# Optimization experiments

Hardware: AMD Instinct MI355X
Metric: run time of the kernel (lower is better)

Reference implementation:

```python
import jax, jax.numpy as jnp
import numpy as np

B, S, E, C = 128, 256, 768, 4


def setup_inputs() -> dict:
    key = jax.random.key(0)
    ks = jax.random.split(key, 8)
    questions = jax.random.normal(ks[0], (B, E), dtype=jnp.float32)
    segments = jax.random.normal(ks[1], (B, S, E), dtype=jnp.float32)
    W1 = jax.random.normal(ks[2], (2 * E, E), dtype=jnp.float32) * 0.02
    b1 = jnp.zeros((E,), dtype=jnp.float32)
    W2 = jax.random.normal(ks[3], (E, E // 2), dtype=jnp.float32) * 0.02
    b2 = jnp.zeros((E // 2,), dtype=jnp.float32)
    W3 = jax.random.normal(ks[4], (E // 2, C), dtype=jnp.float32) * 0.02
    b3 = jnp.zeros((C,), dtype=jnp.float32)
    num_segments = jax.random.randint(ks[5], (B,), 1, S + 1, dtype=jnp.int32)
    return {"questions": questions, "segments": segments, "W1": W1, "b1": b1,
            "W2": W2, "b2": b2, "W3": W3, "b3": b3, "num_segments": num_segments}


def reference(questions, segments, W1, b1, W2, b2, W3, b3, num_segments):
    # --- MLP instance scores (call()): concat question emb with every segment emb ---
    q = jnp.broadcast_to(questions[:, None, :], segments.shape)      # [B,S,E]
    x = jnp.concatenate([q, segments], axis=-1)                      # [B,S,2E]
    h = jax.nn.gelu(x @ W1 + b1, approximate=False)                  # keras gelu is exact
    h = jax.nn.gelu(h @ W2 + b2, approximate=False)
    preds = jax.nn.softmax(h @ W3 + b3, axis=-1)                     # [B,S,C]

    # --- per-bag noisy-OR style aggregation (aggregate_loss inner math, vectorized) ---
    # In the TF code, for class cid: s_j = sum(preds[j,:cid]) (exclusive cumsum over
    # classes), and product_of_sum_prob ACCUMULATES across the i loop, so
    # update_i = preds[i,cid] * cumprod_i( prod_{j!=k} s_j ) (leave-one-out products).
    mask = jnp.arange(S)[None, :] < num_segments[:, None]            # [B,S]
    mC = mask[..., None]                                             # [B,S,1]
    s = jnp.cumsum(preds, axis=-1) - preds                           # exclusive cumsum, [B,S,C]
    s_m = jnp.where(mC, s, 1.0)                                      # padded -> multiplicative identity
    # leave-one-out product over the segment axis via prefix/suffix cumprods
    cp_f = jnp.cumprod(s_m, axis=1)
    prefix = jnp.concatenate([jnp.ones_like(s_m[:, :1]), cp_f[:, :-1]], axis=1)
    cp_b = jnp.cumprod(s_m[:, ::-1], axis=1)[:, ::-1]
    suffix = jnp.concatenate([cp_b[:, 1:], jnp.ones_like(s_m[:, :1])], axis=1)
    L = prefix * suffix                                              # prod_{j!=k} s_j, [B,S,C]
    cpL = jnp.cumprod(L, axis=1)                                     # running product over i (padding is at the end)
    sum_term = jnp.sum(jnp.where(mC, preds * cpL, 0.0), axis=1)      # [B,C]
    prod_term = jnp.prod(jnp.where(mC, preds, 1.0), axis=1)          # prod_i preds[i,cid]
    agg = sum_term / jnp.float32(C) + prod_term                      # bag_pred_agg_scores, [B,C]
    return agg
```

## Files before the change

### kernel.cpp

```cpp
#include <hip/hip_runtime.h>
#include <hip/hip_bf16.h>


typedef __attribute__((ext_vector_type(8))) short short8;
typedef __attribute__((ext_vector_type(8))) unsigned short ushort8;
typedef __attribute__((ext_vector_type(16))) float f32x16;
typedef __attribute__((ext_vector_type(8))) int i32x8;
typedef __attribute__((ext_vector_type(4))) int i32x4;

__device__ __forceinline__ unsigned short f2bf(float f) {
    union { float f; unsigned int u; } c; c.f = f;
    unsigned int u = c.u;
    unsigned int r = (u + 0x7FFFu + ((u >> 16) & 1u)) >> 16;
    return (unsigned short)r;
}
__device__ __forceinline__ float bf2f(unsigned short u) {
    union { unsigned int u; float f; } c; c.u = ((unsigned int)u) << 16;
    return c.f;
}
__device__ __forceinline__ float gelu_fast(float x) {
    float x2 = x * x;
    float y2 = 1.5957691216057308f * (x + 0.044715f * x2 * x);
    float e = __expf(y2);
    float t = 1.0f - 2.0f * __builtin_amdgcn_rcpf(e + 1.0f);
    return 0.5f * x * (1.0f + t);
}

typedef const __attribute__((address_space(1))) void* gas_t;
typedef __attribute__((address_space(3))) void* las_t;
__device__ __forceinline__ void g2l16(const void* g, void* l) {
    __builtin_amdgcn_global_load_lds((gas_t)g, (las_t)l, 16, 0, 0);
}

__device__ __forceinline__ unsigned int f4_to_fp8x4(float a, float b, float c, float d) {
    int lo = __builtin_amdgcn_cvt_pk_fp8_f32(a, b, 0, 0);
    return (unsigned int)__builtin_amdgcn_cvt_pk_fp8_f32(c, d, lo, 1);
}
__device__ __forceinline__ unsigned char f_to_fp8(float a) {
    return (unsigned char)(__builtin_amdgcn_cvt_pk_fp8_f32(a, a, 0, 0) & 0xFF);
}

#define PREP_Q    96
#define PREP_TR1E 240
#define PREP_TR2E 312
#define PREP_END  12600

__global__ __launch_bounds__(256) void prep_kernel(
    const float* __restrict__ segments, unsigned char* __restrict__ segF8,
    const float* __restrict__ W1, unsigned char* __restrict__ W1t8,
    const float* __restrict__ W2, unsigned char* __restrict__ W2t8,
    const float* __restrict__ questions, float* __restrict__ qW1p)
{
    __shared__ __align__(16) char sh[16640];
    const int bid = blockIdx.x, tid = threadIdx.x;

    if (bid < PREP_Q) {
        const int s = bid / 24, rem = bid % 24;
        const int n0 = (rem % 12) * 64, m0 = (rem / 12) * 64;
        float (*As)[64] = (float(*)[64])sh;
        float (*Bs)[64] = (float(*)[64])(sh + 4096);
        const int tn = tid & 15, tm = tid >> 4;
        float acc[4][4] = {};
        const int la_m = tid >> 2;
        const int la_k = (tid & 3) << 2;
        const int lb_k = tid >> 4;
        const int lb_n = (tid & 15) << 2;
        const float* Aptr = questions + (size_t)(m0 + la_m) * 768 + la_k;
        const float* Bptr = W1 + (size_t)lb_k * 768 + n0 + lb_n;
        const int kbeg = s * 192, kend = kbeg + 192;
        for (int k0 = kbeg; k0 < kend; k0 += 16) {
            float4 av = *(const float4*)(Aptr + k0);
            float4 bv = *(const float4*)(Bptr + (size_t)k0 * 768);
            As[la_k + 0][la_m] = av.x;
            As[la_k + 1][la_m] = av.y;
            As[la_k + 2][la_m] = av.z;
            As[la_k + 3][la_m] = av.w;
            *(float4*)&Bs[lb_k][lb_n] = bv;
            __syncthreads();
            #pragma unroll
            for (int k = 0; k < 16; k++) {
                float4 a = *(const float4*)&As[k][tm << 2];
                float4 b = *(const float4*)&Bs[k][tn << 2];
                float ar[4] = {a.x, a.y, a.z, a.w};
                float br[4] = {b.x, b.y, b.z, b.w};
                #pragma unroll
                for (int i = 0; i < 4; i++)
                    #pragma unroll
                    for (int j = 0; j < 4; j++)
                        acc[i][j] += ar[i] * br[j];
            }
            __syncthreads();
        }
        float* outp = qW1p + (size_t)s * 128 * 768;
        #pragma unroll
        for (int i = 0; i < 4; i++) {
            int row = m0 + (tm << 2) + i;
            int colBase = n0 + (tn << 2);
            *(float4*)&outp[(size_t)row * 768 + colBase] =
                make_float4(acc[i][0], acc[i][1], acc[i][2], acc[i][3]);
        }
        return;
    }

    if (bid < PREP_TR2E) {
        const float* in; unsigned char* outp; int R, C, bx, by;
        if (bid < PREP_TR1E) {
            int idx = bid - PREP_Q; bx = idx % 12; by = idx / 12;
            in = W1 + 768 * 768; outp = W1t8; R = 768; C = 768;
        } else {
            int idx = bid - PREP_TR1E; bx = idx % 6; by = idx / 6;
            in = W2; outp = W2t8; R = 768; C = 384;
        }
        float (*t)[65] = (float(*)[65])sh;
        int r0 = by * 64, c0 = bx * 64;
        int tx = tid & 63, ty = tid >> 6;
        #pragma unroll
        for (int p = 0; p < 16; p++) {
            int row = ty * 16 + p;
            t[row][tx] = in[(size_t)(r0 + row) * C + c0 + tx];
        }
        __syncthreads();
        #pragma unroll
        for (int p = 0; p < 16; p++) {
            int orow = ty * 16 + p;
            outp[(size_t)(c0 + orow) * R + r0 + tx] = f_to_fp8(t[tx][orow]);
        }
        return;
    }

    {
        long i = (long)(bid - PREP_TR2E) * 256 + tid;
        const float4* in = (const float4*)segments;
        float4 a = in[2 * i], b = in[2 * i + 1];
        unsigned int lo = f4_to_fp8x4(a.x, a.y, a.z, a.w);
        unsigned int hi = f4_to_fp8x4(b.x, b.y, b.z, b.w);
        *(uint2*)(segF8 + i * 8) = make_uint2(lo, hi);
    }
}

template<int OUT8>
__global__ __launch_bounds__(256) void mfma_gemm_f8(
    const unsigned char* __restrict__ A8,
    const unsigned char* __restrict__ Bt8,
    const float* __restrict__ bias,
    const float* __restrict__ rowAdd,
    void* __restrict__ CoutV,
    int M, int N, int K)
{
    __shared__ __align__(16) unsigned char smem8[32768];
    unsigned char* As = smem8;
    unsigned char* Bs = smem8 + 8192;
    const int tid = threadIdx.x;
    const int wave = tid >> 6, lane = tid & 63;
    const int m0 = blockIdx.y * 128, n0 = blockIdx.x * 128;
    const int wm = (wave & 1) * 64, wn = (wave >> 1) * 64;

    f32x16 acc[2][2] = {};

    const int srow = tid >> 2;
    const int schunk = (tid & 3) ^ ((srow >> 1) & 3);
    const unsigned char* Ag = A8 + (size_t)(m0 + srow) * K + schunk * 16;
    const unsigned char* Bg = Bt8 + (size_t)(n0 + srow) * K + schunk * 16;
    unsigned char* Al = As + tid * 16;
    unsigned char* Bl = Bs + tid * 16;

    const int fm = lane & 31, fq = lane >> 5;

    for (int k0 = 0; k0 < K; k0 += 64) {
        g2l16(Ag + k0, Al);
        g2l16(Ag + (size_t)64 * K + k0, Al + 4096);
        g2l16(Bg + k0, Bl);
        g2l16(Bg + (size_t)64 * K + k0, Bl + 4096);
        __syncthreads();

        i32x8 av[2], bv[2];
        #pragma unroll
        for (int i = 0; i < 2; i++) {
            int rw = wm + i * 32 + fm, key = (rw >> 1) & 3;
            i32x4 lo = *(const i32x4*)&As[rw * 64 + (((fq << 1) | 0) ^ key) * 16];
            i32x4 hi = *(const i32x4*)&As[rw * 64 + (((fq << 1) | 1) ^ key) * 16];
            av[i][0] = lo[0]; av[i][1] = lo[1]; av[i][2] = lo[2]; av[i][3] = lo[3];
            av[i][4] = hi[0]; av[i][5] = hi[1]; av[i][6] = hi[2]; av[i][7] = hi[3];
        }
        #pragma unroll
        for (int j = 0; j < 2; j++) {
            int rw = wn + j * 32 + fm, key = (rw >> 1) & 3;
            i32x4 lo = *(const i32x4*)&Bs[rw * 64 + (((fq << 1) | 0) ^ key) * 16];
            i32x4 hi = *(const i32x4*)&Bs[rw * 64 + (((fq << 1) | 1) ^ key) * 16];
            bv[j][0] = lo[0]; bv[j][1] = lo[1]; bv[j][2] = lo[2]; bv[j][3] = lo[3];
            bv[j][4] = hi[0]; bv[j][5] = hi[1]; bv[j][6] = hi[2]; bv[j][7] = hi[3];
        }
        #pragma unroll
        for (int i = 0; i < 2; i++)
            #pragma unroll
            for (int j = 0; j < 2; j++)
                acc[i][j] = __builtin_amdgcn_mfma_scale_f32_32x32x64_f8f6f4(
                    av[i], bv[j], acc[i][j], 0, 0,
                    0, 127, 0, 127);
        __syncthreads();
    }

    #pragma unroll
    for (int j = 0; j < 2; j++) {
        int coll = wn + j * 32 + fm;
        int col = n0 + coll;
        float add = bias[col];
        if (rowAdd) {
            const float* radd = rowAdd + (size_t)(m0 >> 8) * N;
            add += radd[col] + radd[col + 98304] +
                   radd[col + 2 * 98304] + radd[col + 3 * 98304];
        }
        #pragma unroll
        for (int i = 0; i < 2; i++) {
            int rbase = wm + i * 32 + 4 * fq;
            #pragma unroll
            for (int reg = 0; reg < 16; reg++) {
                int rowl = rbase + (reg & 3) + 8 * (reg >> 2);
                float v = gelu_fast(acc[i][j][reg] + add);
                if (OUT8) smem8[rowl * 128 + coll] = f_to_fp8(v);
                else ((unsigned short*)smem8)[rowl * 128 + coll] = f2bf(v);
            }
        }
    }
    __syncthreads();
    if (OUT8) {
        unsigned char* Cout = (unsigned char*)CoutV;
        #pragma unroll
        for (int it = 0; it < 4; it++) {
            int idx = it * 256 + tid;
            int r = idx >> 3, cc = (idx & 7) * 16;
            *(uint4*)&Cout[(size_t)(m0 + r) * N + n0 + cc] =
                *(const uint4*)&smem8[r * 128 + cc];
        }
    } else {
        unsigned short* Cout = (unsigned short*)CoutV;
        #pragma unroll
        for (int it = 0; it < 8; it++) {
            int idx = it * 256 + tid;
            int r = idx >> 4, cc = (idx & 15) * 8;
            *(ushort8*)&Cout[(size_t)(m0 + r) * N + n0 + cc] =
                *(const ushort8*)&((unsigned short*)smem8)[r * 128 + cc];
        }
    }
}

__device__ __forceinline__ float4 f4mul(float4 a, float4 b) {
    return make_float4(a.x * b.x, a.y * b.y, a.z * b.z, a.w * b.w);
}
__device__ float4 scan_prod(float4 v, float4* buf, int tid) {
    __syncthreads();
    buf[tid] = v;
    __syncthreads();
    #pragma unroll
    for (int off = 1; off < 256; off <<= 1) {
        float4 o = (tid >= off) ? buf[tid - off] : make_float4(1.f, 1.f, 1.f, 1.f);
        __syncthreads();
        v = f4mul(v, o);
        buf[tid] = v;
        __syncthreads();
    }
    return v;
}

__global__ __launch_bounds__(256) void head_kernel(
    const unsigned short* __restrict__ H2, const float* __restrict__ W3,
    const float* __restrict__ b3, const int* __restrict__ nseg,
    float* __restrict__ out)
{
    __shared__ float4 buf[256];
    __shared__ float4 w3s[384];
    const int b = blockIdx.x, tid = threadIdx.x;
    for (int i = tid; i < 384; i += 256) w3s[i] = ((const float4*)W3)[i];
    __syncthreads();

    const unsigned short* hrow = H2 + (size_t)(b * 256 + tid) * 384;
    float4 acc = make_float4(b3[0], b3[1], b3[2], b3[3]);
    #pragma unroll
    for (int kk = 0; kk < 48; kk++) {
        ushort8 u = *(const ushort8*)(hrow + kk * 8);
        #pragma unroll
        for (int j = 0; j < 8; j++) {
            float h = bf2f(u[j]);
            float4 w = w3s[kk * 8 + j];
            acc.x += h * w.x; acc.y += h * w.y; acc.z += h * w.z; acc.w += h * w.w;
        }
    }
    float m = fmaxf(fmaxf(acc.x, acc.y), fmaxf(acc.z, acc.w));
    float e0 = __expf(acc.x - m), e1 = __expf(acc.y - m),
          e2 = __expf(acc.z - m), e3 = __expf(acc.w - m);
    float inv = 1.0f / (e0 + e1 + e2 + e3);
    float4 p = make_float4(e0 * inv, e1 * inv, e2 * inv, e3 * inv);

    const int n = nseg[b];
    const float4 ones = make_float4(1.f, 1.f, 1.f, 1.f);
    bool msk = tid < n;
    float s1 = p.x, s2 = s1 + p.y, s3 = s2 + p.z;
    float4 sm = msk ? make_float4(0.f, s1, s2, s3) : ones;

    scan_prod(sm, buf, tid);
    float4 pfx = (tid > 0) ? buf[tid - 1] : ones;
    __syncthreads();

    buf[255 - tid] = sm;
    __syncthreads();
    float4 rsm = buf[tid];
    scan_prod(rsm, buf, tid);
    float4 sfx = (tid < 255) ? buf[254 - tid] : ones;

    float4 L = f4mul(pfx, sfx);
    float4 cpL = scan_prod(L, buf, tid);

    float4 term = msk ? f4mul(p, cpL) : make_float4(0.f, 0.f, 0.f, 0.f);
    float4 pm = msk ? p : ones;

    __syncthreads();
    buf[tid] = term;
    __syncthreads();
    for (int off = 128; off > 0; off >>= 1) {
        if (tid < off) {
            float4 a = buf[tid], c = buf[tid + off];
            buf[tid] = make_float4(a.x + c.x, a.y + c.y, a.z + c.z, a.w + c.w);
        }
        __syncthreads();
    }
    float4 sum_t = buf[0];
    __syncthreads();

    buf[tid] = pm;
    __syncthreads();
    for (int off = 128; off > 0; off >>= 1) {
        if (tid < off) buf[tid] = f4mul(buf[tid], buf[tid + off]);
        __syncthreads();
    }
    if (tid == 0) {
        float4 pr = buf[0];
        ((float4*)out)[b] = make_float4(0.25f * sum_t.x + pr.x,
                                        0.25f * sum_t.y + pr.y,
                                        0.25f * sum_t.z + pr.z,
                                        0.25f * sum_t.w + pr.w);
    }
}

extern "C" void kernel_launch(void* const* d_in, const int* in_sizes, int n_in,
                              void* d_out, int out_size, void* d_ws, size_t ws_size,
                              hipStream_t stream) {
    (void)in_sizes; (void)n_in; (void)out_size; (void)ws_size;
    const float* questions = (const float*)d_in[0];
    const float* segments  = (const float*)d_in[1];
    const float* W1 = (const float*)d_in[2];
    const float* b1 = (const float*)d_in[3];
    const float* W2 = (const float*)d_in[4];
    const float* b2 = (const float*)d_in[5];
    const float* W3 = (const float*)d_in[6];
    const float* b3 = (const float*)d_in[7];
    const int*  nseg = (const int*)d_in[8];
    float* out = (float*)d_out;

    char* w = (char*)d_ws;
    float* qW1p = (float*)w;                   w += (size_t)4 * 128 * 768 * 4;
    unsigned char*  W1t8 = (unsigned char*)w;  w += (size_t)768 * 768;
    unsigned char*  W2t8 = (unsigned char*)w;  w += (size_t)384 * 768;
    unsigned char*  segF8 = (unsigned char*)w; w += (size_t)32768 * 768;
    unsigned char*  H1f8 = (unsigned char*)w;  w += (size_t)32768 * 768;
    unsigned short* H2b  = (unsigned short*)w; w += (size_t)32768 * 384 * 2;

    prep_kernel<<<PREP_END, 256, 0, stream>>>(
        segments, segF8, W1, W1t8, W2, W2t8, questions, qW1p);
    mfma_gemm_f8<1><<<dim3(6, 256), 256, 0, stream>>>(
        segF8, W1t8, b1, qW1p, H1f8, 32768, 768, 768);
    mfma_gemm_f8<0><<<dim3(3, 256), 256, 0, stream>>>(
        H1f8, W2t8, b2, nullptr, H2b, 32768, 384, 768);
    head_kernel<<<128, 256, 0, stream>>>(H2b, W3, b3, nseg, out);
}
```

Baseline: 247.7 us.

## Fuse W3 projection into second GEMM epilogue and use wave-shuffle scans in head

The second GEMM now multiplies its bf16 output tile by the matching slice of W3 inside the epilogue and writes per-column-block partial logits (3 partials of 4 floats per row) instead of the full 32768x384 bf16 H2 matrix. The head kernel sums the three partials and no longer reads H2 or performs the 384-long dot products. The shared-memory Hillis-Steele product scans and tree reductions are replaced with wave shuffle scans and reductions plus a small cross-wave combine, cutting barriers. In exchange, the GEMM epilogue gains extra LDS reads and FMAs per block.

Result: no change. 243.9 us (-1.5%).

```diff
diff --git a/kernel.cpp b/kernel.cpp
--- a/kernel.cpp
+++ b/kernel.cpp
@@ -138,22 +138,28 @@
     }
 }
 
-template<int OUT8>
+template<int MODE>
 __global__ __launch_bounds__(256) void mfma_gemm_f8(
     const unsigned char* __restrict__ A8,
     const unsigned char* __restrict__ Bt8,
     const float* __restrict__ bias,
     const float* __restrict__ rowAdd,
     void* __restrict__ CoutV,
-    int M, int N, int K)
+    int M, int N, int K,
+    const float* __restrict__ W3p)
 {
-    __shared__ __align__(16) unsigned char smem8[32768];
+    __shared__ __align__(16) unsigned char smem8[32768 + (MODE == 2 ? 2048 : 0)];
     unsigned char* As = smem8;
     unsigned char* Bs = smem8 + 8192;
     const int tid = threadIdx.x;
     const int wave = tid >> 6, lane = tid & 63;
     const int m0 = blockIdx.y * 128, n0 = blockIdx.x * 128;
     const int wm = (wave & 1) * 64, wn = (wave >> 1) * 64;
+
+    if constexpr (MODE == 2) {
+        if (tid < 128)
+            ((float4*)(smem8 + 32768))[tid] = ((const float4*)W3p)[n0 + tid];
+    }
 
     f32x16 acc[2][2] = {};
 
@@ -217,13 +223,13 @@
             for (int reg = 0; reg < 16; reg++) {
                 int rowl = rbase + (reg & 3) + 8 * (reg >> 2);
                 float v = gelu_fast(acc[i][j][reg] + add);
-                if (OUT8) smem8[rowl * 128 + coll] = f_to_fp8(v);
+                if constexpr (MODE == 1) smem8[rowl * 128 + coll] = f_to_fp8(v);
                 else ((unsigned short*)smem8)[rowl * 128 + coll] = f2bf(v);
             }
         }
     }
     __syncthreads();
-    if (OUT8) {
+    if constexpr (MODE == 1) {
         unsigned char* Cout = (unsigned char*)CoutV;
         #pragma unroll
         for (int it = 0; it < 4; it++) {
@@ -232,6 +238,28 @@
             *(uint4*)&Cout[(size_t)(m0 + r) * N + n0 + cc] =
                 *(const uint4*)&smem8[r * 128 + cc];
         }
+    } else if constexpr (MODE == 2) {
+        const float4* w3sh = (const float4*)(smem8 + 32768);
+        const unsigned short* tile = (const unsigned short*)smem8;
+        int r = tid >> 1, ch = tid & 1;
+        const unsigned short* rowp = tile + r * 128 + ch * 64;
+        float4 a = make_float4(0.f, 0.f, 0.f, 0.f);
+        #pragma unroll
+        for (int k = 0; k < 8; k++) {
+            int kk = k ^ (r & 7);
+            ushort8 u = *(const ushort8*)(rowp + kk * 8);
+            #pragma unroll
+            for (int jj = 0; jj < 8; jj++) {
+                float h = bf2f(u[jj]);
+                float4 wv2 = w3sh[ch * 64 + kk * 8 + jj];
+                a.x += h * wv2.x; a.y += h * wv2.y;
+                a.z += h * wv2.z; a.w += h * wv2.w;
+            }
+        }
+        a.x += __shfl_xor(a.x, 1); a.y += __shfl_xor(a.y, 1);
+        a.z += __shfl_xor(a.z, 1); a.w += __shfl_xor(a.w, 1);
+        if (ch == 0)
+            ((float4*)CoutV)[(size_t)blockIdx.x * 32768 + m0 + r] = a;
     } else {
         unsigned short* Cout = (unsigned short*)CoutV;
         #pragma unroll
@@ -247,44 +275,45 @@
 __device__ __forceinline__ float4 f4mul(float4 a, float4 b) {
     return make_float4(a.x * b.x, a.y * b.y, a.z * b.z, a.w * b.w);
 }
-__device__ float4 scan_prod(float4 v, float4* buf, int tid) {
-    __syncthreads();
-    buf[tid] = v;
-    __syncthreads();
+
+__device__ __forceinline__ float4 block_scan_prod(float4 v, int lane, int wv,
+                                                  float4* wtot) {
     #pragma unroll
-    for (int off = 1; off < 256; off <<= 1) {
-        float4 o = (tid >= off) ? buf[tid - off] : make_float4(1.f, 1.f, 1.f, 1.f);
-        __syncthreads();
-        v = f4mul(v, o);
-        buf[tid] = v;
-        __syncthreads();
-    }
-    return v;
+    for (int off = 1; off < 64; off <<= 1) {
+        float4 t;
+        t.x = __shfl_up(v.x, off); t.y = __shfl_up(v.y, off);
+        t.z = __shfl_up(v.z, off); t.w = __shfl_up(v.w, off);
+        if (lane >= off) v = f4mul(v, t);
+    }
+    if (lane == 63) wtot[wv] = v;
+    __syncthreads();
+    float4 pre = make_float4(1.f, 1.f, 1.f, 1.f);
+    #pragma unroll
+    for (int w = 0; w < 3; w++)
+        if (w < wv) pre = f4mul(pre, wtot[w]);
+    __syncthreads();
+    return f4mul(pre, v);
 }
 
 __global__ __launch_bounds__(256) void head_kernel(
-    const unsigned short* __restrict__ H2, const float* __restrict__ W3,
-    const float* __restrict__ b3, const int* __restrict__ nseg,
+    const float* __restrict__ pp,
+    const float* __restrict__ b3,
+    const int* __restrict__ nseg,
     float* __restrict__ out)
 {
-    __shared__ float4 buf[256];
-    __shared__ float4 w3s[384];
+    __shared__ float4 xbuf[256];
+    __shared__ float4 wtot[4];
     const int b = blockIdx.x, tid = threadIdx.x;
-    for (int i = tid; i < 384; i += 256) w3s[i] = ((const float4*)W3)[i];
-    __syncthreads();
-
-    const unsigned short* hrow = H2 + (size_t)(b * 256 + tid) * 384;
-    float4 acc = make_float4(b3[0], b3[1], b3[2], b3[3]);
-    #pragma unroll
-    for (int kk = 0; kk < 48; kk++) {
-        ushort8 u = *(const ushort8*)(hrow + kk * 8);
-        #pragma unroll
-        for (int j = 0; j < 8; j++) {
-            float h = bf2f(u[j]);
-            float4 w = w3s[kk * 8 + j];
-            acc.x += h * w.x; acc.y += h * w.y; acc.z += h * w.z; acc.w += h * w.w;
-        }
-    }
+    const int lane = tid & 63, wv = tid >> 6;
+    const float4 ones = make_float4(1.f, 1.f, 1.f, 1.f);
+
+    const float4* ppv = (const float4*)pp;
+    size_t row = (size_t)b * 256 + tid;
+    float4 a0 = ppv[row], a1 = ppv[row + 32768], a2 = ppv[row + 65536];
+    float4 acc = make_float4(a0.x + a1.x + a2.x + b3[0],
+                             a0.y + a1.y + a2.y + b3[1],
+                             a0.z + a1.z + a2.z + b3[2],
+                             a0.w + a1.w + a2.w + b3[3]);
     float m = fmaxf(fmaxf(acc.x, acc.y), fmaxf(acc.z, acc.w));
     float e0 = __expf(acc.x - m), e1 = __expf(acc.y - m),
           e2 = __expf(acc.z - m), e3 = __expf(acc.w - m);
@@ -292,52 +321,53 @@
     float4 p = make_float4(e0 * inv, e1 * inv, e2 * inv, e3 * inv);
 
     const int n = nseg[b];
-    const float4 ones = make_float4(1.f, 1.f, 1.f, 1.f);
     bool msk = tid < n;
     float s1 = p.x, s2 = s1 + p.y, s3 = s2 + p.z;
     float4 sm = msk ? make_float4(0.f, s1, s2, s3) : ones;
 
-    scan_prod(sm, buf, tid);
-    float4 pfx = (tid > 0) ? buf[tid - 1] : ones;
-    __syncthreads();
-
-    buf[255 - tid] = sm;
-    __syncthreads();
-    float4 rsm = buf[tid];
-    scan_prod(rsm, buf, tid);
-    float4 sfx = (tid < 255) ? buf[254 - tid] : ones;
+    float4 isc = block_scan_prod(sm, lane, wv, wtot);
+    xbuf[tid] = isc;
+    __syncthreads();
+    float4 pfx = (tid > 0) ? xbuf[tid - 1] : ones;
+    __syncthreads();
+
+    xbuf[255 - tid] = sm;
+    __syncthreads();
+    float4 rsm = xbuf[tid];
+    __syncthreads();
+    float4 risc = block_scan_prod(rsm, lane, wv, wtot);
+    xbuf[tid] = risc;
+    __syncthreads();
+    float4 sfx = (tid < 255) ? xbuf[254 - tid] : ones;
+    __syncthreads();
 
     float4 L = f4mul(pfx, sfx);
-    float4 cpL = scan_prod(L, buf, tid);
+    float4 cpL = block_scan_prod(L, lane, wv, wtot);
 
     float4 term = msk ? f4mul(p, cpL) : make_float4(0.f, 0.f, 0.f, 0.f);
     float4 pm = msk ? p : ones;
-
-    __syncthreads();
-    buf[tid] = term;
-    __syncthreads();
-    for (int off = 128; off > 0; off >>= 1) {
-        if (tid < off) {
-            float4 a = buf[tid], c = buf[tid + off];
-            buf[tid] = make_float4(a.x + c.x, a.y + c.y, a.z + c.z, a.w + c.w);
-        }
-        __syncthreads();
-    }
-    float4 sum_t = buf[0];
-    __syncthreads();
-
-    buf[tid] = pm;
-    __syncthreads();
-    for (int off = 128; off > 0; off >>= 1) {
-        if (tid < off) buf[tid] = f4mul(buf[tid], buf[tid + off]);
-        __syncthreads();
-    }
+    #pragma unroll
+    for (int off = 32; off > 0; off >>= 1) {
+        term.x += __shfl_xor(term.x, off); term.y += __shfl_xor(term.y, off);
+        term.z += __shfl_xor(term.z, off); term.w += __shfl_xor(term.w, off);
+        pm.x *= __shfl_xor(pm.x, off); pm.y *= __shfl_xor(pm.y, off);
+        pm.z *= __shfl_xor(pm.z, off); pm.w *= __shfl_xor(pm.w, off);
+    }
+    if (lane == 0) { xbuf[wv] = term; xbuf[4 + wv] = pm; }
+    __syncthreads();
     if (tid == 0) {
-        float4 pr = buf[0];
-        ((float4*)out)[b] = make_float4(0.25f * sum_t.x + pr.x,
-                                        0.25f * sum_t.y + pr.y,
-                                        0.25f * sum_t.z + pr.z,
-                                        0.25f * sum_t.w + pr.w);
+        float4 st = make_float4(0.f, 0.f, 0.f, 0.f);
+        float4 pr = ones;
+        #pragma unroll
+        for (int w = 0; w < 4; w++) {
+            float4 t = xbuf[w], q = xbuf[4 + w];
+            st.x += t.x; st.y += t.y; st.z += t.z; st.w += t.w;
+            pr = f4mul(pr, q);
+        }
+        ((float4*)out)[b] = make_float4(0.25f * st.x + pr.x,
+                                        0.25f * st.y + pr.y,
+                                        0.25f * st.z + pr.z,
+                                        0.25f * st.w + pr.w);
     }
 }
 
@@ -362,13 +392,13 @@
     unsigned char*  W2t8 = (unsigned char*)w;  w += (size_t)384 * 768;
     unsigned char*  segF8 = (unsigned char*)w; w += (size_t)32768 * 768;
     unsigned char*  H1f8 = (unsigned char*)w;  w += (size_t)32768 * 768;
-    unsigned short* H2b  = (unsigned short*)w; w += (size_t)32768 * 384 * 2;
+    float* ppreds = (float*)w;                 w += (size_t)3 * 32768 * 4 * 4;
 
     prep_kernel<<<PREP_END, 256, 0, stream>>>(
         segments, segF8, W1, W1t8, W2, W2t8, questions, qW1p);
     mfma_gemm_f8<1><<<dim3(6, 256), 256, 0, stream>>>(
-        segF8, W1t8, b1, qW1p, H1f8, 32768, 768, 768);
-    mfma_gemm_f8<0><<<dim3(3, 256), 256, 0, stream>>>(
-        H1f8, W2t8, b2, nullptr, H2b, 32768, 384, 768);
-    head_kernel<<<128, 256, 0, stream>>>(H2b, W3, b3, nseg, out);
-}
+        segF8, W1t8, b1, qW1p, H1f8, 32768, 768, 768, nullptr);
+    mfma_gemm_f8<2><<<dim3(3, 256), 256, 0, stream>>>(
+        H1f8, W2t8, b2, nullptr, ppreds, 32768, 384, 768, W3);
+    head_kernel<<<128, 256, 0, stream>>>(ppreds, b3, nseg, out);
+}
```
